# Optimization experiments

Hardware: AMD Instinct MI355X
Metric: run time of the kernel (lower is better)

## Reference

```python
import jax, jax.numpy as jnp
import numpy as np

N_HEAD = 16
NEG_INF = -1e9  # matches the original's -1000000000.0 mask fill


def setup_inputs() -> dict:
    key = jax.random.key(0)
    k1, k2, k3 = jax.random.split(key, 3)
    n_embd = 1024
    b, t = 2, 2048
    x = jax.random.normal(k1, (b, t, n_embd), dtype=jnp.float32)
    w_attn = jax.random.normal(k2, (n_embd, 3 * n_embd), dtype=jnp.float32) * 0.02
    b_attn = jnp.zeros((3 * n_embd,), dtype=jnp.float32)
    w_proj = jax.random.normal(k3, (n_embd, n_embd), dtype=jnp.float32) * 0.02
    b_proj = jnp.zeros((n_embd,), dtype=jnp.float32)
    return {"x": x, "w_attn": w_attn, "b_attn": b_attn, "w_proj": w_proj, "b_proj": b_proj}


def reference(x, w_attn, b_attn, w_proj, b_proj):
    b, t, c = x.shape
    hd = c // N_HEAD
    scale = 1.0 / np.sqrt(hd)
    qkv = x @ w_attn + b_attn                        # [b, t, 3c]
    q, k, v = jnp.split(qkv, 3, axis=-1)
    # split heads -> [b, nh, t, hd]
    def heads(z):
        return z.reshape(b, t, N_HEAD, hd).transpose(0, 2, 1, 3)
    q, k, v = heads(q), heads(k), heads(v)
    att = jnp.einsum('bhqd,bhkd->bhqk', q, k) * scale  # [b, nh, t, t]
    mask = jnp.tril(jnp.ones((t, t), dtype=bool))
    att = jnp.where(mask[None, None], att, jnp.float32(NEG_INF))
    att = jax.nn.softmax(att, axis=-1)
    y = jnp.einsum('bhqk,bhkd->bhqd', att, v)          # [b, nh, t, hd]
    y = y.transpose(0, 2, 1, 3).reshape(b, t, c)
    return y @ w_proj + b_proj
```

## Files before the change

### kernel.cpp

```cpp
#include <hip/hip_runtime.h>
#include <hip/hip_bf16.h>
#include <math.h>

typedef __attribute__((ext_vector_type(8))) short short8;
typedef __attribute__((ext_vector_type(4))) float f32x4;
typedef unsigned short u16;

static __device__ __forceinline__ u16 f2bf(float f) {
  union { float f; unsigned u; } v; v.f = f;
  unsigned r = v.u + 0x7fffu + ((v.u >> 16) & 1u);
  return (u16)(r >> 16);
}

static __device__ __forceinline__ float bf2f(u16 h) {
  union { unsigned u; float f; } v; v.u = ((unsigned)h) << 16;
  return v.f;
}

static __device__ __forceinline__ void gload_lds16(const void* g, void* l) {
  __builtin_amdgcn_global_load_lds(
      (const __attribute__((address_space(1))) void*)g,
      (__attribute__((address_space(3))) void*)l, 16, 0, 0);
}

__global__ __launch_bounds__(256) void cvt_bf16(const float* __restrict__ in,
                                                u16* __restrict__ out, int n) {
  int i = (blockIdx.x * 256 + threadIdx.x) * 8;
  if (i >= n) return;
  float4 a = *(const float4*)(in + i);
  float4 b = *(const float4*)(in + i + 4);
  uint4 pk;
  pk.x = f2bf(a.x) | ((unsigned)f2bf(a.y) << 16);
  pk.y = f2bf(a.z) | ((unsigned)f2bf(a.w) << 16);
  pk.z = f2bf(b.x) | ((unsigned)f2bf(b.y) << 16);
  pk.w = f2bf(b.z) | ((unsigned)f2bf(b.w) << 16);
  *(uint4*)(out + i) = pk;
}

template<int KD, int ND>
__global__ __launch_bounds__(256) void transpose_bf16(const float* __restrict__ W,
                                                      u16* __restrict__ WT) {
  __shared__ float tile[64][65];
  const int c0 = blockIdx.x * 64;
  const int k0 = blockIdx.y * 64;
  const int t = threadIdx.x;
  const int lr = t >> 2;
  const int lc = (t & 3) * 16;
  const float* src = W + (size_t)(k0 + lr) * ND + c0 + lc;
#pragma unroll
  for (int i = 0; i < 16; i += 4) {
    float4 v = *(const float4*)(src + i);
    tile[lr][lc + i] = v.x; tile[lr][lc + i + 1] = v.y;
    tile[lr][lc + i + 2] = v.z; tile[lr][lc + i + 3] = v.w;
  }
  __syncthreads();
  unsigned pk[8];
#pragma unroll
  for (int j = 0; j < 8; ++j) {
    u16 lo = f2bf(tile[lc + 2 * j][lr]);
    u16 hi = f2bf(tile[lc + 2 * j + 1][lr]);
    pk[j] = lo | ((unsigned)hi << 16);
  }
  u16* dst = WT + (size_t)(c0 + lr) * KD + k0 + lc;
  *(uint4*)(dst) = make_uint4(pk[0], pk[1], pk[2], pk[3]);
  *(uint4*)(dst + 8) = make_uint4(pk[4], pk[5], pk[6], pk[7]);
}

template<int NSIZE, int MODE>
__global__ __launch_bounds__(256) void gemm_bt(const u16* __restrict__ A,
                                               const u16* __restrict__ Bt,
                                               const float* __restrict__ bias,
                                               u16* __restrict__ qb,
                                               u16* __restrict__ kb,
                                               u16* __restrict__ vb,
                                               float* __restrict__ outp) {
  constexpr int K = 1024;
  __shared__ u16 As[2][128 * 64];
  __shared__ u16 Bs[2][128 * 64];
  const int tid = threadIdx.x;
  const int lane = tid & 63;
  const int wid = tid >> 6;
  const int l15 = lane & 15;
  const int g4 = lane >> 4;
  const int wm = (wid >> 1) * 64;
  const int wn = (wid & 1) * 64;
  const int row0 = blockIdx.x * 128;
  const int col0 = blockIdx.y * 128;

  f32x4 acc[4][4] = {};

  const int srow = tid >> 3;
  const int sblk = (tid & 7) ^ (srow & 7);
  const u16* ga = A + (size_t)(row0 + srow) * K + sblk * 8;
  const u16* gb = Bt + (size_t)(col0 + srow) * K + sblk * 8;

#pragma unroll
  for (int i = 0; i < 4; ++i) {
    gload_lds16(ga + (size_t)i * 32 * K, As[0] + tid * 8 + i * 2048);
    gload_lds16(gb + (size_t)i * 32 * K, Bs[0] + tid * 8 + i * 2048);
  }

  int cur = 0;
  for (int kt = 0; kt < K / 64; ++kt) {
    if (kt + 1 < K / 64) {
#pragma unroll
      for (int i = 0; i < 4; ++i) {
        gload_lds16(ga + (size_t)i * 32 * K + (kt + 1) * 64, As[cur ^ 1] + tid * 8 + i * 2048);
        gload_lds16(gb + (size_t)i * 32 * K + (kt + 1) * 64, Bs[cur ^ 1] + tid * 8 + i * 2048);
      }
      asm volatile("s_waitcnt vmcnt(8)" ::: "memory");
    } else {
      asm volatile("s_waitcnt vmcnt(0)" ::: "memory");
    }
    __builtin_amdgcn_s_barrier();
    asm volatile("" ::: "memory");

    const u16* Ac = As[cur];
    const u16* Bc = Bs[cur];
#pragma unroll
    for (int ks = 0; ks < 2; ++ks) {
      short8 af[4], bf[4];
      const int B = ks * 64 + g4 * 16;
      const int sw = (l15 & 7) << 4;
#pragma unroll
      for (int mt = 0; mt < 4; ++mt)
        af[mt] = *(const short8*)((const char*)Ac + (wm + mt * 16 + l15) * 128 + (B ^ sw));
#pragma unroll
      for (int nt = 0; nt < 4; ++nt)
        bf[nt] = *(const short8*)((const char*)Bc + (wn + nt * 16 + l15) * 128 + (B ^ sw));
#pragma unroll
      for (int mt = 0; mt < 4; ++mt)
#pragma unroll
        for (int nt = 0; nt < 4; ++nt)
          acc[mt][nt] = __builtin_amdgcn_mfma_f32_16x16x32_bf16(af[mt], bf[nt], acc[mt][nt], 0, 0, 0);
    }

    asm volatile("" ::: "memory");
    __builtin_amdgcn_s_barrier();
    cur ^= 1;
  }

#pragma unroll
  for (int nt = 0; nt < 4; ++nt) {
    const int col = col0 + wn + nt * 16 + l15;
    const float bv = bias[col];
    if (MODE == 0) {
      const int part = col >> 10;
      const int h = (col >> 6) & 15;
      const int d = col & 63;
      u16* dp = part == 0 ? qb : kb;
#pragma unroll
      for (int mt = 0; mt < 4; ++mt) {
        if (part == 2) {
          const int t0 = row0 + wm + mt * 16 + g4 * 4;
          const int bidx = t0 >> 11;
          const int tt = t0 & 2047;
          const unsigned lo = f2bf(acc[mt][nt][0] + bv) | ((unsigned)f2bf(acc[mt][nt][1] + bv) << 16);
          const unsigned hi = f2bf(acc[mt][nt][2] + bv) | ((unsigned)f2bf(acc[mt][nt][3] + bv) << 16);
          *(uint2*)&vb[((size_t)((bidx << 4) + h) * 64 + d) * 2048 + tt] = make_uint2(lo, hi);
        } else {
#pragma unroll
          for (int r = 0; r < 4; ++r) {
            const int row = row0 + wm + mt * 16 + g4 * 4 + r;
            const int bidx = row >> 11;
            const int tt = row & 2047;
            dp[((size_t)((bidx << 4) + h) * 2048 + tt) * 64 + d] = f2bf(acc[mt][nt][r] + bv);
          }
        }
      }
    } else {
#pragma unroll
      for (int mt = 0; mt < 4; ++mt) {
#pragma unroll
        for (int r = 0; r < 4; ++r) {
          const int row = row0 + wm + mt * 16 + g4 * 4 + r;
          outp[(size_t)row * NSIZE + col] = acc[mt][nt][r] + bv;
        }
      }
    }
  }
}

__global__ __launch_bounds__(256, 3) void attn_fwd(const u16* __restrict__ Qb,
                                                   const u16* __restrict__ Kb,
                                                   const u16* __restrict__ Vtb,
                                                   u16* __restrict__ Yb,
                                                   char* __restrict__ pb) {
  __shared__ u16 Ks[2][64 * 64];
  __shared__ u16 Vs[2][64 * 64];
  __shared__ u16 Ps[4][2048];
  const int bh = blockIdx.x;
  const int y = blockIdx.y;
  int j, c0t, c1t, chunk, split;
  if (y < 8)       { j = 8 + y;  c0t = 0;  c1t = 15;        chunk = 0; split = 1; }
  else if (y < 16) { j = 15 - y; c0t = 0;  c1t = 2 * j + 1; chunk = 0; split = 0; }
  else             { j = y - 8;  c0t = 16; c1t = 2 * j + 1; chunk = 1; split = 1; }
  const int q0 = j * 128;
  const int tid = threadIdx.x;
  const int lane = tid & 63;
  const int wid = tid >> 6;
  const int l15 = lane & 15;
  const int g4 = lane >> 4;
  const size_t bhq = (size_t)bh * 2048 * 64;
  const u16* Kbase = Kb + bhq;
  const u16* Vbase = Vtb + bhq;
  const float C2 = 0.18033688011112042f;
  u16* Pw = &Ps[wid][0];
  const int wrow0 = q0 + wid * 32;

  short8 ones;
#pragma unroll
  for (int i = 0; i < 8; ++i) ones[i] = (short)0x3F80;

  short8 qf[2][2];
#pragma unroll
  for (int g = 0; g < 2; ++g) {
    const u16* qp = Qb + bhq + (size_t)(wrow0 + g * 16 + l15) * 64 + g4 * 8;
    qf[g][0] = *(const short8*)(qp);
    qf[g][1] = *(const short8*)(qp + 32);
  }
  f32x4 accy[2][4] = {};
  float m_q[2] = {-1e30f, -1e30f};
  float m_r[2][4] = {{-1e30f, -1e30f, -1e30f, -1e30f}, {-1e30f, -1e30f, -1e30f, -1e30f}};
  float l_r[2][4] = {};

  int cur = 0;
#pragma unroll
  for (int cc = 0; cc < 2; ++cc) {
    const int c = tid + cc * 256;
    const int srow = c >> 3;
    const int sblk = (c & 7) ^ (srow & 7);
    gload_lds16(Kbase + (size_t)(c0t * 64 + srow) * 64 + sblk * 8, Ks[0] + c * 8);
    gload_lds16(Vbase + (size_t)srow * 2048 + c0t * 64 + sblk * 8, Vs[0] + c * 8);
  }

  for (int kv = c0t; kv <= c1t; ++kv) {
    const int kv0 = kv * 64;
    if (kv < c1t) {
      const int nx0 = kv0 + 64;
#pragma unroll
      for (int cc = 0; cc < 2; ++cc) {
        const int c = tid + cc * 256;
        const int srow = c >> 3;
        const int sblk = (c & 7) ^ (srow & 7);
        gload_lds16(Kbase + (size_t)(nx0 + srow) * 64 + sblk * 8, Ks[cur ^ 1] + c * 8);
        gload_lds16(Vbase + (size_t)srow * 2048 + nx0 + sblk * 8, Vs[cur ^ 1] + c * 8);
      }
      asm volatile("s_waitcnt vmcnt(4)" ::: "memory");
    } else {
      asm volatile("s_waitcnt vmcnt(0)" ::: "memory");
    }
    __builtin_amdgcn_s_barrier();
    asm volatile("" ::: "memory");

    if (kv0 <= wrow0 + 31) {
      const u16* Kt = Ks[cur];
      const u16* Vt = Vs[cur];

      f32x4 s[2][4];
#pragma unroll
      for (int nt = 0; nt < 4; ++nt) {
        const int R = nt * 16 + l15;
        const int sw = (R & 7) << 4;
        short8 kf0 = *(const short8*)((const char*)Kt + R * 128 + ((g4 * 16) ^ sw));
        short8 kf1 = *(const short8*)((const char*)Kt + R * 128 + ((64 + g4 * 16) ^ sw));
        f32x4 z0 = __builtin_amdgcn_mfma_f32_16x16x32_bf16(kf0, qf[0][0], f32x4{}, 0, 0, 0);
        s[0][nt] = __builtin_amdgcn_mfma_f32_16x16x32_bf16(kf1, qf[0][1], z0, 0, 0, 0);
        f32x4 z1 = __builtin_amdgcn_mfma_f32_16x16x32_bf16(kf0, qf[1][0], f32x4{}, 0, 0, 0);
        s[1][nt] = __builtin_amdgcn_mfma_f32_16x16x32_bf16(kf1, qf[1][1], z1, 0, 0, 0);
      }

#pragma unroll
      for (int g = 0; g < 2; ++g) {
        const int grow0 = wrow0 + g * 16;
        if (kv0 + 63 > grow0) {
          const int qg = grow0 + l15;
#pragma unroll
          for (int nt = 0; nt < 4; ++nt) {
            const int kbase = kv0 + nt * 16 + g4 * 4;
#pragma unroll
            for (int r = 0; r < 4; ++r)
              if (kbase + r > qg) s[g][nt][r] = -1e30f;
          }
        }
        float mx = fmaxf(fmaxf(fmaxf(s[g][0][0], s[g][0][1]), fmaxf(s[g][0][2], s[g][0][3])),
                         fmaxf(fmaxf(s[g][1][0], s[g][1][1]), fmaxf(s[g][1][2], s[g][1][3])));
        mx = fmaxf(mx, fmaxf(fmaxf(fmaxf(s[g][2][0], s[g][2][1]), fmaxf(s[g][2][2], s[g][2][3])),
                             fmaxf(fmaxf(s[g][3][0], s[g][3][1]), fmaxf(s[g][3][2], s[g][3][3]))));
        mx = fmaxf(mx, __shfl_xor(mx, 16));
        mx = fmaxf(mx, __shfl_xor(mx, 32));
        if (!__all(mx <= m_q[g] + 44.0f)) {
          m_q[g] = fmaxf(m_q[g], mx);
#pragma unroll
          for (int rr = 0; rr < 4; ++rr) {
            const float mn = __shfl(m_q[g], g4 * 4 + rr);
            const float al = __builtin_amdgcn_exp2f((m_r[g][rr] - mn) * C2);
            m_r[g][rr] = mn;
            l_r[g][rr] *= al;
#pragma unroll
            for (int nt = 0; nt < 4; ++nt) accy[g][nt][rr] *= al;
          }
        }
        const float m2 = m_q[g] * C2;
#pragma unroll
        for (int nt = 0; nt < 4; ++nt)
#pragma unroll
          for (int r = 0; r < 4; ++r)
            s[g][nt][r] = __builtin_amdgcn_exp2f(fmaf(s[g][nt][r], C2, -m2));

#pragma unroll
        for (int nt = 0; nt < 4; ++nt) {
          const unsigned lo = f2bf(s[g][nt][0]) | ((unsigned)f2bf(s[g][nt][1]) << 16);
          const unsigned hi = f2bf(s[g][nt][2]) | ((unsigned)f2bf(s[g][nt][3]) << 16);
          const int rowL = g * 16 + l15;
          const int colB = nt * 32 + g4 * 8;
          *(uint2*)((char*)Pw + rowL * 128 + (colB ^ ((rowL & 7) << 4))) = make_uint2(lo, hi);
        }
      }

      short8 pf[2][2];
#pragma unroll
      for (int g = 0; g < 2; ++g) {
        const int rowL = g * 16 + l15;
        const int sw = (rowL & 7) << 4;
        pf[g][0] = *(const short8*)((const char*)Pw + rowL * 128 + ((g4 * 16) ^ sw));
        pf[g][1] = *(const short8*)((const char*)Pw + rowL * 128 + ((64 + g4 * 16) ^ sw));
      }
#pragma unroll
      for (int g = 0; g < 2; ++g) {
        f32x4 ps = __builtin_amdgcn_mfma_f32_16x16x32_bf16(pf[g][0], ones, f32x4{}, 0, 0, 0);
        ps = __builtin_amdgcn_mfma_f32_16x16x32_bf16(pf[g][1], ones, ps, 0, 0, 0);
#pragma unroll
        for (int rr = 0; rr < 4; ++rr) l_r[g][rr] += ps[rr];
      }
#pragma unroll
      for (int nt = 0; nt < 4; ++nt) {
        const int R = nt * 16 + l15;
        const int sw = (R & 7) << 4;
        short8 vf0 = *(const short8*)((const char*)Vt + R * 128 + ((g4 * 16) ^ sw));
        short8 vf1 = *(const short8*)((const char*)Vt + R * 128 + ((64 + g4 * 16) ^ sw));
#pragma unroll
        for (int g = 0; g < 2; ++g) {
          accy[g][nt] = __builtin_amdgcn_mfma_f32_16x16x32_bf16(pf[g][0], vf0, accy[g][nt], 0, 0, 0);
          accy[g][nt] = __builtin_amdgcn_mfma_f32_16x16x32_bf16(pf[g][1], vf1, accy[g][nt], 0, 0, 0);
        }
      }
    }

    asm volatile("" ::: "memory");
    __builtin_amdgcn_s_barrier();
    cur ^= 1;
  }

  if (!split) {
#pragma unroll
    for (int g = 0; g < 2; ++g)
#pragma unroll
      for (int r = 0; r < 4; ++r) {
        const int row = wrow0 + g * 16 + g4 * 4 + r;
        const float inv = 1.0f / l_r[g][r];
        const size_t base = ((size_t)(bh >> 4) * 2048 + row) * 1024 + (bh & 15) * 64;
#pragma unroll
        for (int nt = 0; nt < 4; ++nt)
          Yb[base + nt * 16 + l15] = f2bf(accy[g][nt][r] * inv);
      }
  } else {
    char* slot = pb + ((size_t)(bh * 8 + (j - 8)) * 2 + chunk) * 17408;
    u16* O = (u16*)slot;
    float* mf = (float*)(slot + 16384);
    float* lf = (float*)(slot + 16896);
#pragma unroll
    for (int g = 0; g < 2; ++g)
#pragma unroll
      for (int r = 0; r < 4; ++r) {
        const int row = wid * 32 + g * 16 + g4 * 4 + r;
        const float inv = 1.0f / l_r[g][r];
#pragma unroll
        for (int nt = 0; nt < 4; ++nt)
          O[row * 64 + nt * 16 + l15] = f2bf(accy[g][nt][r] * inv);
        if (l15 == 0) { mf[row] = m_r[g][r]; lf[row] = l_r[g][r]; }
      }
  }
}

__global__ __launch_bounds__(256) void attn_combine(const char* __restrict__ pb,
                                                    u16* __restrict__ Yb) {
  const int x = blockIdx.x;
  const int bh = blockIdx.y;
  const int j = 8 + (x >> 1);
  const int half = x & 1;
  const int T = 2 * j + half;
  const char* s0 = pb + ((size_t)(bh * 8 + (j - 8)) * 2) * 17408;
  const char* s1 = s0 + 17408;
  const int tid = threadIdx.x;
  const int r64 = tid >> 2;
  const int rowl = half * 64 + r64;
  const int dc = (tid & 3) * 16;
  const float C2 = 0.18033688011112042f;
  const float m0 = ((const float*)(s0 + 16384))[rowl];
  const float m1 = ((const float*)(s1 + 16384))[rowl];
  const float l0 = ((const float*)(s0 + 16896))[rowl];
  const float l1 = ((const float*)(s1 + 16896))[rowl];
  const float m = fmaxf(m0, m1);
  const float w0 = __builtin_amdgcn_exp2f((m0 - m) * C2) * l0;
  const float w1 = __builtin_amdgcn_exp2f((m1 - m) * C2) * l1;
  const float inv = 1.0f / (w0 + w1);
  const float a0 = w0 * inv, a1 = w1 * inv;
  const u16* O0 = (const u16*)s0 + rowl * 64 + dc;
  const u16* O1 = (const u16*)s1 + rowl * 64 + dc;
  const int qrow = T * 64 + r64;
  u16* yp = Yb + ((size_t)(bh >> 4) * 2048 + qrow) * 1024 + (bh & 15) * 64 + dc;
  union { uint4 v; u16 h[8]; } a[2], b[2], o[2];
  a[0].v = *(const uint4*)O0; a[1].v = *(const uint4*)(O0 + 8);
  b[0].v = *(const uint4*)O1; b[1].v = *(const uint4*)(O1 + 8);
#pragma unroll
  for (int jj = 0; jj < 2; ++jj)
#pragma unroll
    for (int i = 0; i < 8; ++i)
      o[jj].h[i] = f2bf(bf2f(a[jj].h[i]) * a0 + bf2f(b[jj].h[i]) * a1);
  *(uint4*)yp = o[0].v;
  *(uint4*)(yp + 8) = o[1].v;
}

extern "C" void kernel_launch(void* const* d_in, const int* in_sizes, int n_in,
                              void* d_out, int out_size, void* d_ws, size_t ws_size,
                              hipStream_t stream) {
  const float* x      = (const float*)d_in[0];
  const float* w_attn = (const float*)d_in[1];
  const float* b_attn = (const float*)d_in[2];
  const float* w_proj = (const float*)d_in[3];
  const float* b_proj = (const float*)d_in[4];
  float* out = (float*)d_out;
  char* ws = (char*)d_ws;

  u16* xb  = (u16*)(ws + (size_t)0);
  u16* wTa = (u16*)(ws + ((size_t)8  << 20));
  u16* wTp = (u16*)(ws + ((size_t)14 << 20));
  u16* qb  = (u16*)(ws + ((size_t)16 << 20));
  u16* kb  = (u16*)(ws + ((size_t)24 << 20));
  u16* vb  = (u16*)(ws + ((size_t)32 << 20));
  u16* yb  = (u16*)(ws + ((size_t)40 << 20));
  char* pb = ws;

  cvt_bf16<<<2048, 256, 0, stream>>>(x, xb, 2 * 2048 * 1024);
  transpose_bf16<1024, 3072><<<dim3(48, 16), 256, 0, stream>>>(w_attn, wTa);
  transpose_bf16<1024, 1024><<<dim3(16, 16), 256, 0, stream>>>(w_proj, wTp);
  gemm_bt<3072, 0><<<dim3(32, 24), 256, 0, stream>>>(xb, wTa, b_attn, qb, kb, vb, nullptr);
  attn_fwd<<<dim3(32, 24), 256, 0, stream>>>(qb, kb, vb, yb, pb);
  attn_combine<<<dim3(16, 32), 256, 0, stream>>>(pb, yb);
  gemm_bt<1024, 1><<<dim3(32, 8), 256, 0, stream>>>(yb, wTp, b_proj, nullptr, nullptr, nullptr, out);
}
```

Baseline: 123.0 us.

## Fuse prologue conversion kernels and switch GEMM to single-buffered 128-wide K tiles

Merges the x-to-bf16 conversion and both weight transpose kernels into one launch, with each block dispatched by its block index, to remove two kernel launch gaps. Separately, the GEMM drops double-buffered 64-wide K tiles in favour of a single 128-wide K tile per iteration with a 16-chunk XOR swizzle. This halves the number of barriers per K loop but removes the overlap of global loads with MFMA compute, since each tile now waits on vmcnt(0) before computing. LDS use per block stays the same.

Measured after the change: 113.8 us. -7.5%, faster.

```diff
diff --git a/kernel.cpp b/kernel.cpp
--- a/kernel.cpp
+++ b/kernel.cpp
@@ -23,27 +23,10 @@
       (__attribute__((address_space(3))) void*)l, 16, 0, 0);
 }
 
-__global__ __launch_bounds__(256) void cvt_bf16(const float* __restrict__ in,
-                                                u16* __restrict__ out, int n) {
-  int i = (blockIdx.x * 256 + threadIdx.x) * 8;
-  if (i >= n) return;
-  float4 a = *(const float4*)(in + i);
-  float4 b = *(const float4*)(in + i + 4);
-  uint4 pk;
-  pk.x = f2bf(a.x) | ((unsigned)f2bf(a.y) << 16);
-  pk.y = f2bf(a.z) | ((unsigned)f2bf(a.w) << 16);
-  pk.z = f2bf(b.x) | ((unsigned)f2bf(b.y) << 16);
-  pk.w = f2bf(b.z) | ((unsigned)f2bf(b.w) << 16);
-  *(uint4*)(out + i) = pk;
-}
-
-template<int KD, int ND>
-__global__ __launch_bounds__(256) void transpose_bf16(const float* __restrict__ W,
-                                                      u16* __restrict__ WT) {
-  __shared__ float tile[64][65];
-  const int c0 = blockIdx.x * 64;
-  const int k0 = blockIdx.y * 64;
-  const int t = threadIdx.x;
+__device__ __forceinline__ void transpose_tile(const float* __restrict__ W,
+                                               u16* __restrict__ WT,
+                                               int ND, int KD, int c0, int k0,
+                                               float (*tile)[65], int t) {
   const int lr = t >> 2;
   const int lc = (t & 3) * 16;
   const float* src = W + (size_t)(k0 + lr) * ND + c0 + lc;
@@ -64,6 +47,34 @@
   u16* dst = WT + (size_t)(c0 + lr) * KD + k0 + lc;
   *(uint4*)(dst) = make_uint4(pk[0], pk[1], pk[2], pk[3]);
   *(uint4*)(dst + 8) = make_uint4(pk[4], pk[5], pk[6], pk[7]);
+}
+
+__global__ __launch_bounds__(256) void fused_prologue(const float* __restrict__ x,
+                                                      const float* __restrict__ w_attn,
+                                                      const float* __restrict__ w_proj,
+                                                      u16* __restrict__ xb,
+                                                      u16* __restrict__ wTa,
+                                                      u16* __restrict__ wTp) {
+  __shared__ float tile[64][65];
+  const int b = blockIdx.x;
+  const int t = threadIdx.x;
+  if (b < 2048) {
+    const int i = (b * 256 + t) * 8;
+    float4 a = *(const float4*)(x + i);
+    float4 c = *(const float4*)(x + i + 4);
+    uint4 pk;
+    pk.x = f2bf(a.x) | ((unsigned)f2bf(a.y) << 16);
+    pk.y = f2bf(a.z) | ((unsigned)f2bf(a.w) << 16);
+    pk.z = f2bf(c.x) | ((unsigned)f2bf(c.y) << 16);
+    pk.w = f2bf(c.z) | ((unsigned)f2bf(c.w) << 16);
+    *(uint4*)(xb + i) = pk;
+  } else if (b < 2816) {
+    const int id = b - 2048;
+    transpose_tile(w_attn, wTa, 3072, 1024, (id % 48) * 64, (id / 48) * 64, tile, t);
+  } else {
+    const int id = b - 2816;
+    transpose_tile(w_proj, wTp, 1024, 1024, (id % 16) * 64, (id / 16) * 64, tile, t);
+  }
 }
 
 template<int NSIZE, int MODE>
@@ -75,8 +86,8 @@
                                                u16* __restrict__ vb,
                                                float* __restrict__ outp) {
   constexpr int K = 1024;
-  __shared__ u16 As[2][128 * 64];
-  __shared__ u16 Bs[2][128 * 64];
+  __shared__ u16 As[128 * 128];
+  __shared__ u16 Bs[128 * 128];
   const int tid = threadIdx.x;
   const int lane = tid & 63;
   const int wid = tid >> 6;
@@ -89,45 +100,32 @@
 
   f32x4 acc[4][4] = {};
 
-  const int srow = tid >> 3;
-  const int sblk = (tid & 7) ^ (srow & 7);
-  const u16* ga = A + (size_t)(row0 + srow) * K + sblk * 8;
-  const u16* gb = Bt + (size_t)(col0 + srow) * K + sblk * 8;
-
-#pragma unroll
-  for (int i = 0; i < 4; ++i) {
-    gload_lds16(ga + (size_t)i * 32 * K, As[0] + tid * 8 + i * 2048);
-    gload_lds16(gb + (size_t)i * 32 * K, Bs[0] + tid * 8 + i * 2048);
-  }
-
-  int cur = 0;
-  for (int kt = 0; kt < K / 64; ++kt) {
-    if (kt + 1 < K / 64) {
-#pragma unroll
-      for (int i = 0; i < 4; ++i) {
-        gload_lds16(ga + (size_t)i * 32 * K + (kt + 1) * 64, As[cur ^ 1] + tid * 8 + i * 2048);
-        gload_lds16(gb + (size_t)i * 32 * K + (kt + 1) * 64, Bs[cur ^ 1] + tid * 8 + i * 2048);
-      }
-      asm volatile("s_waitcnt vmcnt(8)" ::: "memory");
-    } else {
-      asm volatile("s_waitcnt vmcnt(0)" ::: "memory");
+  for (int kt = 0; kt < K / 128; ++kt) {
+#pragma unroll
+    for (int cc = 0; cc < 8; ++cc) {
+      const int c = tid + cc * 256;
+      const int row = c >> 4;
+      const int ch = (c & 15) ^ (row & 15);
+      gload_lds16(A + (size_t)(row0 + row) * K + kt * 128 + ch * 8, As + c * 8);
+      gload_lds16(Bt + (size_t)(col0 + row) * K + kt * 128 + ch * 8, Bs + c * 8);
     }
+    asm volatile("s_waitcnt vmcnt(0)" ::: "memory");
     __builtin_amdgcn_s_barrier();
     asm volatile("" ::: "memory");
 
-    const u16* Ac = As[cur];
-    const u16* Bc = Bs[cur];
-#pragma unroll
-    for (int ks = 0; ks < 2; ++ks) {
+#pragma unroll
+    for (int ks = 0; ks < 4; ++ks) {
       short8 af[4], bf[4];
-      const int B = ks * 64 + g4 * 16;
-      const int sw = (l15 & 7) << 4;
-#pragma unroll
-      for (int mt = 0; mt < 4; ++mt)
-        af[mt] = *(const short8*)((const char*)Ac + (wm + mt * 16 + l15) * 128 + (B ^ sw));
-#pragma unroll
-      for (int nt = 0; nt < 4; ++nt)
-        bf[nt] = *(const short8*)((const char*)Bc + (wn + nt * 16 + l15) * 128 + (B ^ sw));
+#pragma unroll
+      for (int mt = 0; mt < 4; ++mt) {
+        const int row = wm + mt * 16 + l15;
+        af[mt] = *(const short8*)((const char*)As + row * 256 + ((((ks * 4 + g4) ^ l15) & 15) << 4));
+      }
+#pragma unroll
+      for (int nt = 0; nt < 4; ++nt) {
+        const int row = wn + nt * 16 + l15;
+        bf[nt] = *(const short8*)((const char*)Bs + row * 256 + ((((ks * 4 + g4) ^ l15) & 15) << 4));
+      }
 #pragma unroll
       for (int mt = 0; mt < 4; ++mt)
 #pragma unroll
@@ -137,7 +135,6 @@
 
     asm volatile("" ::: "memory");
     __builtin_amdgcn_s_barrier();
-    cur ^= 1;
   }
 
 #pragma unroll
@@ -442,9 +439,7 @@
   u16* yb  = (u16*)(ws + ((size_t)40 << 20));
   char* pb = ws;
 
-  cvt_bf16<<<2048, 256, 0, stream>>>(x, xb, 2 * 2048 * 1024);
-  transpose_bf16<1024, 3072><<<dim3(48, 16), 256, 0, stream>>>(w_attn, wTa);
-  transpose_bf16<1024, 1024><<<dim3(16, 16), 256, 0, stream>>>(w_proj, wTp);
+  fused_prologue<<<3072, 256, 0, stream>>>(x, w_attn, w_proj, xb, wTa, wTp);
   gemm_bt<3072, 0><<<dim3(32, 24), 256, 0, stream>>>(xb, wTa, b_attn, qb, kb, vb, nullptr);
   attn_fwd<<<dim3(32, 24), 256, 0, stream>>>(qb, kb, vb, yb, pb);
   attn_combine<<<dim3(16, 32), 256, 0, stream>>>(pb, yb);
```
